# Optimization experiments

Measured on AMD Instinct MI355X. Metric: run time of the kernel, lower is better.

The kernel has to match this reference:

```python
import jax, jax.numpy as jnp
import numpy as np

H, P, T = 256, 16, 4      # hidden_size, maxout_pool_size, max_dec_steps
B, M = 32, 600            # batch, document length

def _lstm_cell(x, h, c, W_ih, W_hh, b_ih, b_hh):
    g = x @ W_ih.T + b_ih + h @ W_hh.T + b_hh
    i, f, gg, o = jnp.split(g, 4, axis=1)  # torch gate order i,f,g,o
    c = jax.nn.sigmoid(f) * c + jax.nn.sigmoid(i) * jnp.tanh(gg)
    h = jax.nn.sigmoid(o) * jnp.tanh(c)
    return h, c

def _maxout(h, U, u_cat, mask_mult, W_lin, W1, b1, W2, b2, W12, b12):
    b, m, _ = U.shape
    r = jnp.tanh(jnp.concatenate([h, u_cat], axis=1) @ W_lin.T)                  # [b,H]
    m1_in = jnp.concatenate([U, jnp.broadcast_to(r[:, None, :], (b, m, H))], 2)  # [b,m,3H]
    m1 = (m1_in @ W1.T + b1).reshape(b, m, H, P).max(-1)                         # [b,m,H]
    m2 = (m1 @ W2.T + b2).reshape(b, m, H, P).max(-1)                            # [b,m,H]
    alpha = (jnp.concatenate([m1, m2], axis=2) @ W12.T + b12).max(-1)            # [b,m]
    return jax.nn.log_softmax(alpha + mask_mult, axis=1)

def _forward(U, d_mask, span, W_ih, W_hh, b_ih, b_hh,
             Ws_lin, Ws_m1, bs_m1, Ws_m2, bs_m2, Ws_m12, bs_m12,
             We_lin, We_m1, be_m1, We_m2, be_m2, We_m12, be_m12):
    b, m, _ = U.shape
    idxb = jnp.arange(b)
    mask_mult = (1.0 - d_mask.astype(U.dtype)) * -1e30
    s_i = jnp.zeros(b, jnp.int32)
    e_i = (jnp.sum(d_mask, 1) - 1).astype(jnp.int32)
    s_tgt, e_tgt = span[:, 0], span[:, 1]
    h = jnp.zeros((b, H), U.dtype)
    c = jnp.zeros((b, H), U.dtype)
    mask_s = mask_e = None
    res_s, res_e, res_ms, res_me, losses = [], [], [], [], []
    u_s = U[idxb, s_i]
    for t in range(T):
        u_e = U[idxb, e_i]
        u_cat = jnp.concatenate([u_s, u_e], axis=1)
        h, c = _lstm_cell(u_cat, h, c, W_ih, W_hh, b_ih, b_hh)
        # start pointer
        lsm = _maxout(h, U, u_cat, mask_mult, Ws_lin, Ws_m1, bs_m1, Ws_m2, bs_m2, Ws_m12, bs_m12)
        idx = jnp.argmax(lsm, axis=1).astype(jnp.int32)
        if t == 0:
            mask_s = jnp.ones(b, bool)
        else:
            idx = idx * mask_s.astype(jnp.int32)
            prev = s_i * mask_s.astype(jnp.int32)
            mask_s = idx != prev
        loss_s = jnp.mean(-jnp.take_along_axis(lsm, s_tgt[:, None], 1)[:, 0]) * mask_s.astype(U.dtype)
        s_i = idx
        u_s = U[idxb, s_i]
        # end pointer
        u_cat2 = jnp.concatenate([u_s, u_e], axis=1)
        lsm_e = _maxout(h, U, u_cat2, mask_mult, We_lin, We_m1, be_m1, We_m2, be_m2, We_m12, be_m12)
        idx_e = jnp.argmax(lsm_e, axis=1).astype(jnp.int32)
        if t == 0:
            mask_e = jnp.ones(b, bool)
        else:
            idx_e = idx_e * mask_e.astype(jnp.int32)
            prev_e = e_i * mask_e.astype(jnp.int32)
            mask_e = idx_e != prev_e
        loss_e = jnp.mean(-jnp.take_along_axis(lsm_e, e_tgt[:, None], 1)[:, 0]) * mask_e.astype(U.dtype)
        e_i = idx_e
        losses.append(loss_s + loss_e)
        res_s.append(s_i); res_ms.append(mask_s)
        res_e.append(e_i); res_me.append(mask_e)
    pos_s = jnp.sum(jnp.stack(res_ms, 1).astype(jnp.int32), 1) - 1
    p1 = jnp.take_along_axis(jnp.stack(res_s, 1), pos_s[:, None], 1)[:, 0]
    pos_e = jnp.sum(jnp.stack(res_me, 1).astype(jnp.int32), 1) - 1
    p2 = jnp.take_along_axis(jnp.stack(res_e, 1), pos_e[:, None], 1)[:, 0]
    loss = jnp.mean(jnp.sum(jnp.stack(losses, 1), 1) / T)
    return loss, p1, p2

def setup_inputs():
    key = jax.random.key(0)
    ks = jax.random.split(key, 16)
    U = jax.random.normal(ks[0], (B, M, 2 * H), jnp.float32)
    lengths = jax.random.randint(ks[1], (B,), M // 2, M + 1)
    d_mask = (jnp.arange(M)[None, :] < lengths[:, None]).astype(jnp.int32)
    span = jax.random.randint(ks[2], (B, 2), 0, M // 2).astype(jnp.int32)
    def w(k, shape, fan_in):
        return (jax.random.normal(k, shape, jnp.float32) / np.float32(np.sqrt(fan_in)))
    b_ih = jnp.zeros(4 * H, jnp.float32).at[H:2 * H].set(1.0)  # forget-gate bias init
    params = {
        'W_ih': w(ks[3], (4 * H, 4 * H), 4 * H), 'W_hh': w(ks[4], (4 * H, H), H),
        'b_ih': b_ih, 'b_hh': jnp.zeros(4 * H, jnp.float32),
        'Ws_lin': w(ks[5], (H, 5 * H), 5 * H),
        'Ws_m1': w(ks[6], (H * P, 3 * H), 3 * H), 'bs_m1': jnp.zeros(H * P, jnp.float32),
        'Ws_m2': w(ks[7], (H * P, H), H), 'bs_m2': jnp.zeros(H * P, jnp.float32),
        'Ws_m12': w(ks[8], (P, 2 * H), 2 * H), 'bs_m12': jnp.zeros(P, jnp.float32),
        'We_lin': w(ks[9], (H, 5 * H), 5 * H),
        'We_m1': w(ks[10], (H * P, 3 * H), 3 * H), 'be_m1': jnp.zeros(H * P, jnp.float32),
        'We_m2': w(ks[11], (H * P, H), H), 'be_m2': jnp.zeros(H * P, jnp.float32),
        'We_m12': w(ks[12], (P, 2 * H), 2 * H), 'be_m12': jnp.zeros(P, jnp.float32),
    }
    return {'U': U, 'd_mask': d_mask, 'span': span, **params}

def reference(U, d_mask, span, W_ih, W_hh, b_ih, b_hh,
              Ws_lin, Ws_m1, bs_m1, Ws_m2, bs_m2, Ws_m12, bs_m12,
              We_lin, We_m1, be_m1, We_m2, be_m2, We_m12, be_m12):
    return _forward(U, d_mask, span, W_ih, W_hh, b_ih, b_hh,
                    Ws_lin, Ws_m1, bs_m1, Ws_m2, bs_m2, Ws_m12, bs_m12,
                    We_lin, We_m1, be_m1, We_m2, be_m2, We_m12, be_m12)
```

## Files before the change

### kernel.cpp

```cpp
#include <hip/hip_runtime.h>
#include <math.h>

namespace {

typedef unsigned short u16;
typedef __attribute__((ext_vector_type(4))) float f32x4;
typedef __attribute__((ext_vector_type(8))) _Float16 f16x8;
typedef __attribute__((ext_vector_type(4))) _Float16 f16x4;

constexpr int B = 32;
constexpr int M = 600;
constexpr int H = 256;
constexpr int TSTEPS = 4;
constexpr int HP = 4096;
constexpr int BM = B * M;
constexpr int TWOH = 512;
constexpr int THREEH = 768;
constexpr int FOURH = 1024;
constexpr int FIVEH = 1280;
constexpr int NTILES = BM / 128;

__device__ __forceinline__ float sigf(float x) { return 1.0f / (1.0f + expf(-x)); }

__device__ __forceinline__ void gload16(const u16* g, u16* l) {
    __builtin_amdgcn_global_load_lds(
        (const __attribute__((address_space(1))) void*)g,
        (__attribute__((address_space(3))) void*)l, 16, 0, 0);
}

__global__ void k_init(const int* __restrict__ d_mask,
                       float* __restrict__ h, float* __restrict__ c,
                       float* __restrict__ loss_vec,
                       int* __restrict__ s_i, int* __restrict__ e_i,
                       int* __restrict__ p1r, int* __restrict__ p2r)
{
    int tid = threadIdx.x;
    for (int i = tid; i < B * H; i += 256) { h[i] = 0.f; c[i] = 0.f; }
    if (tid < B) {
        loss_vec[tid] = 0.f;
        s_i[tid] = 0;
        int s = 0;
        const int* row = d_mask + tid * M;
        for (int m = 0; m < M; ++m) s += row[m];
        e_i[tid] = s - 1;
        p1r[tid] = 0; p2r[tid] = 0;
    }
}

__global__ __launch_bounds__(128) void k_flags(const int* __restrict__ d_mask,
                                               int* __restrict__ flags)
{
    int bm = blockIdx.x * 128 + threadIdx.x;
    int cnt = __syncthreads_count(d_mask[bm]);
    if (threadIdx.x == 0) flags[blockIdx.x] = (cnt == 0) ? 1 : 0;
}

__global__ __launch_bounds__(256) void k_gather(
    const float* __restrict__ U, const int* __restrict__ s_i,
    const int* __restrict__ e_i, float* __restrict__ u_cat)
{
    int idx = blockIdx.x * 256 + threadIdx.x;
    int b = idx >> 9, k = idx & 511;
    u_cat[b * FOURH + k]       = U[((size_t)b * M + s_i[b]) * TWOH + k];
    u_cat[b * FOURH + 512 + k] = U[((size_t)b * M + e_i[b]) * TWOH + k];
}

__global__ __launch_bounds__(256) void k_lstm_gemm(
    const float* __restrict__ u_cat, const float* __restrict__ h,
    const float* __restrict__ W_ih, const float* __restrict__ W_hh,
    const float* __restrict__ b_ih, const float* __restrict__ b_hh,
    float* __restrict__ g)
{
    int idx = blockIdx.x * 256 + threadIdx.x;
    int b = idx >> 10, j = idx & 1023;
    float acc = 0.f;
    const float4* x4 = (const float4*)(u_cat + b * FOURH);
    const float4* wi4 = (const float4*)(W_ih + (size_t)j * FOURH);
    #pragma unroll 4
    for (int k = 0; k < FOURH / 4; ++k) {
        float4 a = x4[k], w = wi4[k];
        acc += a.x * w.x + a.y * w.y + a.z * w.z + a.w * w.w;
    }
    const float4* h4 = (const float4*)(h + b * H);
    const float4* wh4 = (const float4*)(W_hh + (size_t)j * H);
    #pragma unroll 4
    for (int k = 0; k < H / 4; ++k) {
        float4 a = h4[k], w = wh4[k];
        acc += a.x * w.x + a.y * w.y + a.z * w.z + a.w * w.w;
    }
    g[idx] = acc + b_ih[j] + b_hh[j];
}

__global__ __launch_bounds__(256) void k_lstm_gates(
    const float* __restrict__ g, float* __restrict__ h, float* __restrict__ c)
{
    int idx = blockIdx.x * 256 + threadIdx.x;
    int b = idx >> 8, i = idx & (H - 1);
    const float* gr = g + b * FOURH;
    float gi = gr[i], gf = gr[H + i], gg = gr[2 * H + i], go = gr[3 * H + i];
    float cn = sigf(gf) * c[idx] + sigf(gi) * tanhf(gg);
    c[idx] = cn;
    h[idx] = sigf(go) * tanhf(cn);
}

__global__ __launch_bounds__(256) void k_r(
    const float* __restrict__ h, const float* __restrict__ u_cat,
    const float* __restrict__ W_lin, float* __restrict__ r)
{
    int idx = blockIdx.x * 256 + threadIdx.x;
    int b = idx >> 8, i = idx & (H - 1);
    const float* w = W_lin + (size_t)i * FIVEH;
    float acc = 0.f;
    const float4* h4 = (const float4*)(h + b * H);
    const float4* w4 = (const float4*)w;
    #pragma unroll 4
    for (int k = 0; k < H / 4; ++k) {
        float4 a = h4[k], ww = w4[k];
        acc += a.x * ww.x + a.y * ww.y + a.z * ww.z + a.w * ww.w;
    }
    const float4* x4 = (const float4*)(u_cat + b * FOURH);
    const float4* w4b = (const float4*)(w + H);
    #pragma unroll 4
    for (int k = 0; k < FOURH / 4; ++k) {
        float4 a = x4[k], ww = w4b[k];
        acc += a.x * ww.x + a.y * ww.y + a.z * ww.z + a.w * ww.w;
    }
    r[idx] = tanhf(acc);
}

__global__ __launch_bounds__(256) void k_rW(
    const float* __restrict__ r, const float* __restrict__ W1,
    const float* __restrict__ b1, float* __restrict__ rW)
{
    int idx = blockIdx.x * 256 + threadIdx.x;
    int b = idx >> 12, j = idx & (HP - 1);
    const float4* r4 = (const float4*)(r + b * H);
    const float4* w4 = (const float4*)(W1 + (size_t)j * THREEH + TWOH);
    float acc = 0.f;
    #pragma unroll 4
    for (int k = 0; k < H / 4; ++k) {
        float4 a = r4[k], w = w4[k];
        acc += a.x * w.x + a.y * w.y + a.z * w.z + a.w * w.w;
    }
    rW[idx] = acc + b1[j];
}

__global__ __launch_bounds__(256) void k_rW2(
    const float* __restrict__ r, const float* __restrict__ Wt,
    const float* __restrict__ b1, float* __restrict__ rW)
{
    const int b = blockIdx.y;
    const int j = blockIdx.x * 256 + threadIdx.x;
    __shared__ float sr[256];
    sr[threadIdx.x] = r[b * H + threadIdx.x];
    __syncthreads();
    float acc = b1[j];
    #pragma unroll 4
    for (int k = 0; k < H; ++k) acc += sr[k] * Wt[(size_t)k * HP + j];
    rW[(size_t)b * HP + j] = acc;
}

__global__ __launch_bounds__(256) void k_transp(
    const float* __restrict__ W, float* __restrict__ Wt)
{
    int idx = blockIdx.x * 256 + threadIdx.x;
    int k = idx >> 12, j = idx & (HP - 1);
    Wt[idx] = W[(size_t)j * THREEH + TWOH + k];
}

__global__ __launch_bounds__(256) void k_cvtH(
    const float* __restrict__ src, int ld, int Kc, _Float16* __restrict__ dst)
{
    int i4 = blockIdx.x * 256 + threadIdx.x;
    int perrow = Kc >> 2;
    int row = i4 / perrow;
    int kc = (i4 - row * perrow) << 2;
    float4 v = *(const float4*)(src + (size_t)row * ld + kc);
    f16x4 o;
    o[0] = (_Float16)v.x; o[1] = (_Float16)v.y; o[2] = (_Float16)v.z; o[3] = (_Float16)v.w;
    *(f16x4*)(dst + (size_t)row * Kc + kc) = o;
}

template <int EPI>
__global__ __launch_bounds__(256, 4) void gemmJ(
    const _Float16* __restrict__ A, const _Float16* __restrict__ Bw,
    int K, const float* __restrict__ extra, const int* __restrict__ skip,
    float* __restrict__ Cf, _Float16* __restrict__ Ch)
{
    if (skip[blockIdx.y]) return;
    __shared__ __align__(16) u16 sA[2][128 * 32];
    __shared__ __align__(16) u16 sB[2][128 * 32];
    const int tid = threadIdx.x;
    const int w = tid >> 6, lane = tid & 63;
    const int row0 = blockIdx.y * 128, col0 = blockIdx.x * 128;
    const int wm = w & 1, wn = w >> 1;

    const int r1g = tid >> 2,        k1 = (tid & 3) ^ ((r1g >> 1) & 3);
    const int r2g = (tid + 256) >> 2, k2 = ((tid + 256) & 3) ^ ((r2g >> 1) & 3);
    const size_t gA1 = (size_t)(row0 + r1g) * K + k1 * 8;
    const size_t gA2 = (size_t)(row0 + r2g) * K + k2 * 8;
    const size_t gB1 = (size_t)(col0 + r1g) * K + k1 * 8;
    const size_t gB2 = (size_t)(col0 + r2g) * K + k2 * 8;

    f32x4 acc[4][4] = {};

    gload16((const u16*)(A  + gA1), &sA[0][tid * 8]);
    gload16((const u16*)(A  + gA2), &sA[0][(tid + 256) * 8]);
    gload16((const u16*)(Bw + gB1), &sB[0][tid * 8]);
    gload16((const u16*)(Bw + gB2), &sB[0][(tid + 256) * 8]);

    const int iters = K >> 5;
    const int mrow = lane & 15;
    const int kg = lane >> 4;
    const int slot = kg ^ ((mrow >> 1) & 3);
    const int eoff = slot << 3;

    for (int it = 0; it < iters; ++it) {
        const int cur = it & 1;
        __syncthreads();
        if (it + 1 < iters) {
            const int k0n = (it + 1) << 5;
            gload16((const u16*)(A  + gA1 + k0n), &sA[1 - cur][tid * 8]);
            gload16((const u16*)(A  + gA2 + k0n), &sA[1 - cur][(tid + 256) * 8]);
            gload16((const u16*)(Bw + gB1 + k0n), &sB[1 - cur][tid * 8]);
            gload16((const u16*)(Bw + gB2 + k0n), &sB[1 - cur][(tid + 256) * 8]);
        }
        const u16* pa = &sA[cur][(wm * 64 + mrow) * 32 + eoff];
        const u16* pb = &sB[cur][(wn * 64 + mrow) * 32 + eoff];
        f16x8 fa[4], fb[4];
        #pragma unroll
        for (int f = 0; f < 4; ++f) {
            fa[f] = *(const f16x8*)(pa + f * 16 * 32);
            fb[f] = *(const f16x8*)(pb + f * 16 * 32);
        }
        #pragma unroll
        for (int i = 0; i < 4; ++i) {
            #pragma unroll
            for (int j = 0; j < 4; ++j) {
                acc[i][j] = __builtin_amdgcn_mfma_f32_16x16x32_f16(fa[i], fb[j], acc[i][j], 0, 0, 0);
            }
        }
    }

    const int cq = lane & 15, rq = lane >> 4;
    if (EPI == 4) {
        #pragma unroll
        for (int i = 0; i < 4; ++i) {
            #pragma unroll
            for (int j = 0; j < 4; ++j) {
                int col = col0 + wn * 64 + j * 16 + cq;
                #pragma unroll
                for (int rr = 0; rr < 4; ++rr) {
                    int row = row0 + wm * 64 + i * 16 + rq * 4 + rr;
                    Ch[(size_t)row * HP + col] = (_Float16)acc[i][j][rr];
                }
            }
        }
    } else if (EPI == 1) {
        #pragma unroll
        for (int j = 0; j < 4; ++j) {
            int col = col0 + wn * 64 + j * 16 + cq;
            int gcol = (col0 >> 4) + wn * 4 + j;
            float bv = extra[col];
            #pragma unroll
            for (int i = 0; i < 4; ++i) {
                #pragma unroll
                for (int rr = 0; rr < 4; ++rr) {
                    float v = acc[i][j][rr] + bv;
                    v = fmaxf(v, __shfl_xor(v, 1));
                    v = fmaxf(v, __shfl_xor(v, 2));
                    v = fmaxf(v, __shfl_xor(v, 4));
                    v = fmaxf(v, __shfl_xor(v, 8));
                    if (cq == 0) {
                        int row = row0 + wm * 64 + i * 16 + rq * 4 + rr;
                        Cf[(size_t)row * H + gcol] = v;
                    }
                }
            }
        }
    } else {
        #pragma unroll
        for (int j = 0; j < 4; ++j) {
            int col = col0 + wn * 64 + j * 16 + cq;
            int gcol = (col0 >> 4) + wn * 4 + j;
            #pragma unroll
            for (int i = 0; i < 4; ++i) {
                #pragma unroll
                for (int rr = 0; rr < 4; ++rr) {
                    int row = row0 + wm * 64 + i * 16 + rq * 4 + rr;
                    int b = row / M;
                    float v = acc[i][j][rr] + extra[(size_t)b * HP + col];
                    v = fmaxf(v, __shfl_xor(v, 1));
                    v = fmaxf(v, __shfl_xor(v, 2));
                    v = fmaxf(v, __shfl_xor(v, 4));
                    v = fmaxf(v, __shfl_xor(v, 8));
                    if (cq == 0)
                        Ch[(size_t)row * H + gcol] = (_Float16)v;
                }
            }
        }
    }
}

__global__ __launch_bounds__(256) void k_m1A16(
    const _Float16* __restrict__ A, const float* __restrict__ rW,
    _Float16* __restrict__ m1)
{
    int idx = blockIdx.x * 256 + threadIdx.x;
    int bm = idx >> 8;
    int h = idx & (H - 1);
    int b = bm / M;
    const f16x8* a8 = (const f16x8*)(A + (size_t)bm * HP + (h << 4));
    const float4* r4 = (const float4*)(rW + (size_t)b * HP + (h << 4));
    f16x8 a0 = a8[0], a1 = a8[1];
    float4 ra = r4[0], rb = r4[1], rc = r4[2], rd = r4[3];
    float mx;
    mx = fmaxf(fmaxf(fmaxf((float)a0[0] + ra.x, (float)a0[1] + ra.y),
                     fmaxf((float)a0[2] + ra.z, (float)a0[3] + ra.w)),
         fmaxf(fmaxf((float)a0[4] + rb.x, (float)a0[5] + rb.y),
               fmaxf((float)a0[6] + rb.z, (float)a0[7] + rb.w)));
    mx = fmaxf(mx,
         fmaxf(fmaxf(fmaxf((float)a1[0] + rc.x, (float)a1[1] + rc.y),
                     fmaxf((float)a1[2] + rc.z, (float)a1[3] + rc.w)),
               fmaxf(fmaxf((float)a1[4] + rd.x, (float)a1[5] + rd.y),
                     fmaxf((float)a1[6] + rd.z, (float)a1[7] + rd.w))));
    m1[idx] = (_Float16)mx;
}

template <int EPI>
__global__ __launch_bounds__(256) void gemm64(
    const float* __restrict__ Ag, int lda,
    const float* __restrict__ Bg, int ldb,
    const float* __restrict__ extra,
    float* __restrict__ C, int K, int ldc)
{
    __shared__ float As[16][68];
    __shared__ float Bs[16][68];
    const int tid = threadIdx.x;
    const int tx = tid & 15;
    const int ty = tid >> 4;
    const int row0 = blockIdx.y * 64;
    const int col0 = blockIdx.x * 64;
    const int lr = tid >> 2;
    const int lk = (tid & 3) << 2;
    const float* Aload = Ag + (size_t)(row0 + lr) * lda + lk;
    const float* Bload = Bg + (size_t)(col0 + lr) * ldb + lk;
    float acc[4][4] = {};
    for (int k0 = 0; k0 < K; k0 += 16) {
        float4 av = *(const float4*)(Aload + k0);
        float4 bv = *(const float4*)(Bload + k0);
        __syncthreads();
        As[lk + 0][lr] = av.x; As[lk + 1][lr] = av.y; As[lk + 2][lr] = av.z; As[lk + 3][lr] = av.w;
        Bs[lk + 0][lr] = bv.x; Bs[lk + 1][lr] = bv.y; Bs[lk + 2][lr] = bv.z; Bs[lk + 3][lr] = bv.w;
        __syncthreads();
        #pragma unroll
        for (int k = 0; k < 16; ++k) {
            float4 a4 = *(const float4*)(&As[k][ty << 2]);
            float4 b4 = *(const float4*)(&Bs[k][tx << 2]);
            acc[0][0] += a4.x * b4.x; acc[0][1] += a4.x * b4.y; acc[0][2] += a4.x * b4.z; acc[0][3] += a4.x * b4.w;
            acc[1][0] += a4.y * b4.x; acc[1][1] += a4.y * b4.y; acc[1][2] += a4.y * b4.z; acc[1][3] += a4.y * b4.w;
            acc[2][0] += a4.z * b4.x; acc[2][1] += a4.z * b4.y; acc[2][2] += a4.z * b4.z; acc[2][3] += a4.z * b4.w;
            acc[3][0] += a4.w * b4.x; acc[3][1] += a4.w * b4.y; acc[3][2] += a4.w * b4.z; acc[3][3] += a4.w * b4.w;
        }
    }
    if (EPI == 1) {
        const int cb = col0 + (tx << 2);
        float b0 = extra[cb], b1v = extra[cb + 1], b2v = extra[cb + 2], b3v = extra[cb + 3];
        #pragma unroll
        for (int i = 0; i < 4; ++i) {
            float mth = fmaxf(fmaxf(acc[i][0] + b0, acc[i][1] + b1v),
                              fmaxf(acc[i][2] + b2v, acc[i][3] + b3v));
            float r1 = fmaxf(mth, __shfl_xor(mth, 1));
            float r2 = fmaxf(r1, __shfl_xor(r1, 2));
            if ((tx & 3) == 0)
                C[(size_t)(row0 + (ty << 2) + i) * ldc + (col0 >> 4) + (tx >> 2)] = r2;
        }
    } else if (EPI == 2) {
        const int cb = col0 + (tx << 2);
        #pragma unroll
        for (int i = 0; i < 4; ++i) {
            int row = row0 + (ty << 2) + i;
            int b = row / M;
            const float* rw = extra + (size_t)b * HP + cb;
            float mth = fmaxf(fmaxf(acc[i][0] + rw[0], acc[i][1] + rw[1]),
                              fmaxf(acc[i][2] + rw[2], acc[i][3] + rw[3]));
            float r1 = fmaxf(mth, __shfl_xor(mth, 1));
            float r2 = fmaxf(r1, __shfl_xor(r1, 2));
            if ((tx & 3) == 0)
                C[(size_t)row * ldc + (col0 >> 4) + (tx >> 2)] = r2;
        }
    }
}

__global__ __launch_bounds__(256) void k_alpha(
    const float* __restrict__ m1, const float* __restrict__ m2,
    const float* __restrict__ W12, const float* __restrict__ b12,
    const int* __restrict__ d_mask, float* __restrict__ alpha)
{
    __shared__ float Ws[16 * 512];
    const int tid = threadIdx.x;
    for (int i = tid; i < 16 * 512; i += 256) Ws[i] = W12[i];
    __syncthreads();
    const int wave = tid >> 6, lane = tid & 63;
    const int bm = blockIdx.x * 4 + wave;
    const float* r1 = m1 + (size_t)bm * H;
    const float* r2 = m2 + (size_t)bm * H;
    float acc[16] = {};
    #pragma unroll
    for (int q = 0; q < 4; ++q) {
        int k = lane + (q << 6);
        float x = r1[k];
        #pragma unroll
        for (int p = 0; p < 16; ++p) acc[p] += x * Ws[p * 512 + k];
    }
    #pragma unroll
    for (int q = 0; q < 4; ++q) {
        int k = lane + (q << 6);
        float x = r2[k];
        #pragma unroll
        for (int p = 0; p < 16; ++p) acc[p] += x * Ws[p * 512 + 256 + k];
    }
    #pragma unroll
    for (int p = 0; p < 16; ++p) {
        float v = acc[p];
        v += __shfl_xor(v, 1);  v += __shfl_xor(v, 2);  v += __shfl_xor(v, 4);
        v += __shfl_xor(v, 8);  v += __shfl_xor(v, 16); v += __shfl_xor(v, 32);
        acc[p] = v;
    }
    if (lane == 0) {
        float mx = -INFINITY;
        #pragma unroll
        for (int p = 0; p < 16; ++p) mx = fmaxf(mx, acc[p] + b12[p]);
        alpha[bm] = d_mask[bm] ? mx : -1e30f;
    }
}

__global__ __launch_bounds__(256) void k_alpha2(
    const _Float16* __restrict__ m1, const float* __restrict__ m2,
    const float* __restrict__ W12, const float* __restrict__ b12,
    const int* __restrict__ d_mask, float* __restrict__ alpha)
{
    __shared__ float Ws[16 * 512];
    const int tid = threadIdx.x;
    for (int i = tid; i < 16 * 512; i += 256) Ws[i] = W12[i];
    __syncthreads();
    const int wave = tid >> 6, lane = tid & 63;
    const int bm = blockIdx.x * 4 + wave;
    if (!d_mask[bm]) {
        if (lane == 0) alpha[bm] = -1e30f;
        return;
    }
    const _Float16* r1 = m1 + (size_t)bm * H;
    const float* r2 = m2 + (size_t)bm * H;
    float acc[16] = {};
    #pragma unroll
    for (int q = 0; q < 4; ++q) {
        int k = lane + (q << 6);
        float x = (float)r1[k];
        #pragma unroll
        for (int p = 0; p < 16; ++p) acc[p] += x * Ws[p * 512 + k];
    }
    #pragma unroll
    for (int q = 0; q < 4; ++q) {
        int k = lane + (q << 6);
        float x = r2[k];
        #pragma unroll
        for (int p = 0; p < 16; ++p) acc[p] += x * Ws[p * 512 + 256 + k];
    }
    #pragma unroll
    for (int p = 0; p < 16; ++p) {
        float v = acc[p];
        v += __shfl_xor(v, 1);  v += __shfl_xor(v, 2);  v += __shfl_xor(v, 4);
        v += __shfl_xor(v, 8);  v += __shfl_xor(v, 16); v += __shfl_xor(v, 32);
        acc[p] = v;
    }
    if (lane == 0) {
        float mx = -INFINITY;
        #pragma unroll
        for (int p = 0; p < 16; ++p) mx = fmaxf(mx, acc[p] + b12[p]);
        alpha[bm] = mx;
    }
}

__global__ __launch_bounds__(256) void k_softmax(
    const float* __restrict__ alpha, const int* __restrict__ span, int phase,
    float* __restrict__ loss_term, int* __restrict__ idx_out)
{
    __shared__ float sv[256];
    __shared__ int si[256];
    const int b = blockIdx.x, tid = threadIdx.x;
    const float* row = alpha + b * M;
    float best = -INFINITY; int bidx = 0;
    for (int m = tid; m < M; m += 256) {
        float v = row[m];
        if (v > best) { best = v; bidx = m; }
    }
    sv[tid] = best; si[tid] = bidx;
    __syncthreads();
    for (int s = 128; s > 0; s >>= 1) {
        if (tid < s) {
            float v2 = sv[tid + s]; int i2 = si[tid + s];
            if (v2 > sv[tid] || (v2 == sv[tid] && i2 < si[tid])) { sv[tid] = v2; si[tid] = i2; }
        }
        __syncthreads();
    }
    float bmax = sv[0]; int amax = si[0];
    __syncthreads();
    float ps = 0.f;
    for (int m = tid; m < M; m += 256) ps += expf(row[m] - bmax);
    sv[tid] = ps;
    __syncthreads();
    for (int s = 128; s > 0; s >>= 1) {
        if (tid < s) sv[tid] += sv[tid + s];
        __syncthreads();
    }
    if (tid == 0) {
        float lse = bmax + logf(sv[0]);
        int tgt = span[b * 2 + phase];
        loss_term[b] = -(row[tgt] - lse);
        idx_out[b] = amax;
    }
}

__global__ void k_update(const int* __restrict__ idx_in, const float* __restrict__ loss_term,
                         int* __restrict__ pos, int* __restrict__ mask,
                         int* __restrict__ prun, float* __restrict__ loss_vec, int t)
{
    int b = threadIdx.x;
    int active = (b < B) ? 1 : 0;
    int ni = 0, nm = 0;
    if (active) {
        int id = idx_in[b];
        if (t == 0) { nm = 1; ni = id; }
        else {
            int om = mask[b];
            ni = id * om;
            int prev = pos[b] * om;
            nm = (ni != prev) ? 1 : 0;
        }
    }
    float v = active ? loss_term[b] : 0.f;
    #pragma unroll
    for (int off = 32; off > 0; off >>= 1) v += __shfl_xor(v, off);
    float S = v * (1.0f / (float)B);
    if (active) {
        pos[b] = ni;
        mask[b] = nm;
        if (nm) { prun[b] = ni; loss_vec[b] += S; }
    }
}

__global__ void k_finalize(const float* __restrict__ loss_vec, const int* __restrict__ p1r,
                           const int* __restrict__ p2r, float* __restrict__ out)
{
    int b = threadIdx.x;
    float v = (b < B) ? loss_vec[b] : 0.f;
    #pragma unroll
    for (int off = 32; off > 0; off >>= 1) v += __shfl_xor(v, off);
    if (b == 0) out[0] = v / (float)(B * TSTEPS);
    if (b < B) {
        out[1 + b] = (float)p1r[b];
        out[1 + B + b] = (float)p2r[b];
    }
}

}

extern "C" void kernel_launch(void* const* d_in, const int* in_sizes, int n_in,
                              void* d_out, int out_size, void* d_ws, size_t ws_size,
                              hipStream_t stream)
{
    const float* U      = (const float*)d_in[0];
    const int*   d_mask = (const int*)d_in[1];
    const int*   span   = (const int*)d_in[2];
    const float* W_ih   = (const float*)d_in[3];
    const float* W_hh   = (const float*)d_in[4];
    const float* b_ih   = (const float*)d_in[5];
    const float* b_hh   = (const float*)d_in[6];
    const float* Ws_lin = (const float*)d_in[7];
    const float* Ws_m1  = (const float*)d_in[8];
    const float* bs_m1  = (const float*)d_in[9];
    const float* Ws_m2  = (const float*)d_in[10];
    const float* bs_m2  = (const float*)d_in[11];
    const float* Ws_m12 = (const float*)d_in[12];
    const float* bs_m12 = (const float*)d_in[13];
    const float* We_lin = (const float*)d_in[14];
    const float* We_m1  = (const float*)d_in[15];
    const float* be_m1  = (const float*)d_in[16];
    const float* We_m2  = (const float*)d_in[17];
    const float* be_m2  = (const float*)d_in[18];
    const float* We_m12 = (const float*)d_in[19];
    const float* be_m12 = (const float*)d_in[20];

    float* ws = (float*)d_ws;
    size_t o = 0;
    float* m2b   = ws + o; o += (size_t)BM * H;
    float* alphab= ws + o; o += BM;
    float* u_cat = ws + o; o += B * FOURH;
    float* gbuf  = ws + o; o += B * FOURH;
    float* hbuf  = ws + o; o += B * H;
    float* cbuf  = ws + o; o += B * H;
    float* rbuf  = ws + o; o += B * H;
    float* rWb   = ws + o; o += B * HP;
    float* loss_term = ws + o; o += B;
    float* loss_vec  = ws + o; o += B;
    int* ib = (int*)(ws + o); o += 8 * B + 160;
    int* idxb   = ib + 0 * B;
    int* s_i    = ib + 1 * B;
    int* e_i    = ib + 2 * B;
    int* mask_s = ib + 3 * B;
    int* mask_e = ib + 4 * B;
    int* p1r    = ib + 5 * B;
    int* p2r    = ib + 6 * B;
    int* flags  = ib + 8 * B;
    size_t o_common = (o + 3) & ~(size_t)3;

    float* m1b = ws + o_common;

    size_t p = o_common;
    float* Wt_s = ws + p; p += (size_t)H * HP;
    float* Wt_e = ws + p; p += (size_t)H * HP;
    _Float16* hs = (_Float16*)(ws + p);
    size_t q = 0;
    _Float16* Uh  = hs + q; q += (size_t)BM * TWOH;
    _Float16* W1s = hs + q; q += (size_t)HP * TWOH;
    _Float16* W1e = hs + q; q += (size_t)HP * TWOH;
    _Float16* W2s = hs + q; q += (size_t)HP * H;
    _Float16* W2e = hs + q; q += (size_t)HP * H;
    _Float16* m1b16 = hs + q; q += (size_t)BM * H;
    q = (q + 7) & ~(size_t)7;
    const size_t need2 = p * sizeof(float) + q * sizeof(_Float16);
    _Float16* A_s16 = hs + q;
    _Float16* A_e16 = A_s16 + (size_t)BM * HP;
    const size_t need15s = need2 + (size_t)BM * HP * sizeof(_Float16);
    const size_t need16  = need15s + (size_t)BM * HP * sizeof(_Float16);

    const int tier = (ws_size >= need16) ? 16
                   : (ws_size >= need15s) ? 15
                   : (ws_size >= need2) ? 2 : 3;

    k_init<<<1, 256, 0, stream>>>(d_mask, hbuf, cbuf, loss_vec, s_i, e_i, p1r, p2r);

    if (tier != 3) {
        k_flags<<<NTILES, 128, 0, stream>>>(d_mask, flags);
        k_cvtH<<<BM * TWOH / 4 / 256, 256, 0, stream>>>(U, TWOH, TWOH, Uh);
        k_cvtH<<<HP * TWOH / 4 / 256, 256, 0, stream>>>(Ws_m1, THREEH, TWOH, W1s);
        k_cvtH<<<HP * TWOH / 4 / 256, 256, 0, stream>>>(We_m1, THREEH, TWOH, W1e);
        k_cvtH<<<HP * H / 4 / 256, 256, 0, stream>>>(Ws_m2, H, H, W2s);
        k_cvtH<<<HP * H / 4 / 256, 256, 0, stream>>>(We_m2, H, H, W2e);
        k_transp<<<HP * H / 256, 256, 0, stream>>>(Ws_m1, Wt_s);
        k_transp<<<HP * H / 256, 256, 0, stream>>>(We_m1, Wt_e);

        dim3 gJ(HP / 128, NTILES);
        if (tier >= 15) {
            gemmJ<4><<<gJ, 256, 0, stream>>>(Uh, W1s, TWOH, nullptr, flags, nullptr, A_s16);
        }
        if (tier == 16) {
            gemmJ<4><<<gJ, 256, 0, stream>>>(Uh, W1e, TWOH, nullptr, flags, nullptr, A_e16);
        }

        for (int t = 0; t < TSTEPS; ++t) {
            k_gather<<<64, 256, 0, stream>>>(U, s_i, e_i, u_cat);
            k_lstm_gemm<<<128, 256, 0, stream>>>(u_cat, hbuf, W_ih, W_hh, b_ih, b_hh, gbuf);
            k_lstm_gates<<<32, 256, 0, stream>>>(gbuf, hbuf, cbuf);

            k_r<<<32, 256, 0, stream>>>(hbuf, u_cat, Ws_lin, rbuf);
            k_rW2<<<dim3(HP / 256, B), 256, 0, stream>>>(rbuf, Wt_s, bs_m1, rWb);
            if (tier >= 15)
                k_m1A16<<<BM * H / 256, 256, 0, stream>>>(A_s16, rWb, m1b16);
            else
                gemmJ<3><<<gJ, 256, 0, stream>>>(Uh, W1s, TWOH, rWb, flags, nullptr, m1b16);
            gemmJ<1><<<gJ, 256, 0, stream>>>(m1b16, W2s, H, bs_m2, flags, m2b, nullptr);
            k_alpha2<<<BM / 4, 256, 0, stream>>>(m1b16, m2b, Ws_m12, bs_m12, d_mask, alphab);
            k_softmax<<<B, 256, 0, stream>>>(alphab, span, 0, loss_term, idxb);
            k_update<<<1, 64, 0, stream>>>(idxb, loss_term, s_i, mask_s, p1r, loss_vec, t);

            k_gather<<<64, 256, 0, stream>>>(U, s_i, e_i, u_cat);

            k_r<<<32, 256, 0, stream>>>(hbuf, u_cat, We_lin, rbuf);
            k_rW2<<<dim3(HP / 256, B), 256, 0, stream>>>(rbuf, Wt_e, be_m1, rWb);
            if (tier == 16)
                k_m1A16<<<BM * H / 256, 256, 0, stream>>>(A_e16, rWb, m1b16);
            else
                gemmJ<3><<<gJ, 256, 0, stream>>>(Uh, W1e, TWOH, rWb, flags, nullptr, m1b16);
            gemmJ<1><<<gJ, 256, 0, stream>>>(m1b16, W2e, H, be_m2, flags, m2b, nullptr);
            k_alpha2<<<BM / 4, 256, 0, stream>>>(m1b16, m2b, We_m12, be_m12, d_mask, alphab);
            k_softmax<<<B, 256, 0, stream>>>(alphab, span, 1, loss_term, idxb);
            k_update<<<1, 64, 0, stream>>>(idxb, loss_term, e_i, mask_e, p2r, loss_vec, t);
        }
    } else {
        dim3 gemm_grid(HP / 64, BM / 64);
        for (int t = 0; t < TSTEPS; ++t) {
            k_gather<<<64, 256, 0, stream>>>(U, s_i, e_i, u_cat);
            k_lstm_gemm<<<128, 256, 0, stream>>>(u_cat, hbuf, W_ih, W_hh, b_ih, b_hh, gbuf);
            k_lstm_gates<<<32, 256, 0, stream>>>(gbuf, hbuf, cbuf);

            k_r<<<32, 256, 0, stream>>>(hbuf, u_cat, Ws_lin, rbuf);
            k_rW<<<512, 256, 0, stream>>>(rbuf, Ws_m1, bs_m1, rWb);
            gemm64<2><<<gemm_grid, 256, 0, stream>>>(U, TWOH, Ws_m1, THREEH, rWb, m1b, TWOH, H);
            gemm64<1><<<gemm_grid, 256, 0, stream>>>(m1b, H, Ws_m2, H, bs_m2, m2b, H, H);
            k_alpha<<<BM / 4, 256, 0, stream>>>(m1b, m2b, Ws_m12, bs_m12, d_mask, alphab);
            k_softmax<<<B, 256, 0, stream>>>(alphab, span, 0, loss_term, idxb);
            k_update<<<1, 64, 0, stream>>>(idxb, loss_term, s_i, mask_s, p1r, loss_vec, t);

            k_gather<<<64, 256, 0, stream>>>(U, s_i, e_i, u_cat);

            k_r<<<32, 256, 0, stream>>>(hbuf, u_cat, We_lin, rbuf);
            k_rW<<<512, 256, 0, stream>>>(rbuf, We_m1, be_m1, rWb);
            gemm64<2><<<gemm_grid, 256, 0, stream>>>(U, TWOH, We_m1, THREEH, rWb, m1b, TWOH, H);
            gemm64<1><<<gemm_grid, 256, 0, stream>>>(m1b, H, We_m2, H, be_m2, m2b, H, H);
            k_alpha<<<BM / 4, 256, 0, stream>>>(m1b, m2b, We_m12, be_m12, d_mask, alphab);
            k_softmax<<<B, 256, 0, stream>>>(alphab, span, 1, loss_term, idxb);
            k_update<<<1, 64, 0, stream>>>(idxb, loss_term, e_i, mask_e, p2r, loss_vec, t);
        }
    }

    k_finalize<<<1, 64, 0, stream>>>(loss_vec, p1r, p2r, (float*)d_out);
}
```

Baseline: 2.884 ms.

## Fuse gather into LSTM/r kernels, merge softmax+update, batch alpha rows per wave

Removes the separate gather launches by reading the U rows at s_i/e_i directly inside new LSTM-GEMM and r kernels. Softmax, argmax and the pointer/loss update are merged into a single 1024-thread block kernel, one wave per batch row. k_alpha2 now handles four rows per wave, so its launch shrinks and the W12 shared-memory load is spread over more rows. This cuts kernel launches and redundant W12 staging. The cost is a single-block reduction kernel and less parallelism in the alpha kernel.

Result: no change. 2.878 ms (-0.2%).

```diff
diff --git a/kernel.cpp b/kernel.cpp
--- a/kernel.cpp
+++ b/kernel.cpp
@@ -65,6 +65,42 @@
     u_cat[b * FOURH + 512 + k] = U[((size_t)b * M + e_i[b]) * TWOH + k];
 }
 
+__global__ __launch_bounds__(256) void k_lstm_gemm2(
+    const float* __restrict__ U, const int* __restrict__ s_i,
+    const int* __restrict__ e_i, const float* __restrict__ h,
+    const float* __restrict__ W_ih, const float* __restrict__ W_hh,
+    const float* __restrict__ b_ih, const float* __restrict__ b_hh,
+    float* __restrict__ g)
+{
+    int idx = blockIdx.x * 256 + threadIdx.x;
+    int b = idx >> 10, j = idx & 1023;
+    const float* us = U + ((size_t)b * M + s_i[b]) * TWOH;
+    const float* ue = U + ((size_t)b * M + e_i[b]) * TWOH;
+    float acc = 0.f;
+    const float4* x4 = (const float4*)us;
+    const float4* wi4 = (const float4*)(W_ih + (size_t)j * FOURH);
+    #pragma unroll 4
+    for (int k = 0; k < TWOH / 4; ++k) {
+        float4 a = x4[k], w = wi4[k];
+        acc += a.x * w.x + a.y * w.y + a.z * w.z + a.w * w.w;
+    }
+    const float4* y4 = (const float4*)ue;
+    const float4* wi4b = wi4 + TWOH / 4;
+    #pragma unroll 4
+    for (int k = 0; k < TWOH / 4; ++k) {
+        float4 a = y4[k], w = wi4b[k];
+        acc += a.x * w.x + a.y * w.y + a.z * w.z + a.w * w.w;
+    }
+    const float4* h4 = (const float4*)(h + b * H);
+    const float4* wh4 = (const float4*)(W_hh + (size_t)j * H);
+    #pragma unroll 4
+    for (int k = 0; k < H / 4; ++k) {
+        float4 a = h4[k], w = wh4[k];
+        acc += a.x * w.x + a.y * w.y + a.z * w.z + a.w * w.w;
+    }
+    g[idx] = acc + b_ih[j] + b_hh[j];
+}
+
 __global__ __launch_bounds__(256) void k_lstm_gemm(
     const float* __restrict__ u_cat, const float* __restrict__ h,
     const float* __restrict__ W_ih, const float* __restrict__ W_hh,
@@ -101,6 +137,39 @@
     float cn = sigf(gf) * c[idx] + sigf(gi) * tanhf(gg);
     c[idx] = cn;
     h[idx] = sigf(go) * tanhf(cn);
+}
+
+__global__ __launch_bounds__(256) void k_r2(
+    const float* __restrict__ h, const float* __restrict__ U,
+    const int* __restrict__ s_i, const int* __restrict__ e_i,
+    const float* __restrict__ W_lin, float* __restrict__ r)
+{
+    int idx = blockIdx.x * 256 + threadIdx.x;
+    int b = idx >> 8, i = idx & (H - 1);
+    const float* w = W_lin + (size_t)i * FIVEH;
+    float acc = 0.f;
+    const float4* h4 = (const float4*)(h + b * H);
+    const float4* w4 = (const float4*)w;
+    #pragma unroll 4
+    for (int k = 0; k < H / 4; ++k) {
+        float4 a = h4[k], ww = w4[k];
+        acc += a.x * ww.x + a.y * ww.y + a.z * ww.z + a.w * ww.w;
+    }
+    const float4* x4 = (const float4*)(U + ((size_t)b * M + s_i[b]) * TWOH);
+    const float4* w4b = (const float4*)(w + H);
+    #pragma unroll 4
+    for (int k = 0; k < TWOH / 4; ++k) {
+        float4 a = x4[k], ww = w4b[k];
+        acc += a.x * ww.x + a.y * ww.y + a.z * ww.z + a.w * ww.w;
+    }
+    const float4* y4 = (const float4*)(U + ((size_t)b * M + e_i[b]) * TWOH);
+    const float4* w4c = (const float4*)(w + H + TWOH);
+    #pragma unroll 4
+    for (int k = 0; k < TWOH / 4; ++k) {
+        float4 a = y4[k], ww = w4c[k];
+        acc += a.x * ww.x + a.y * ww.y + a.z * ww.z + a.w * ww.w;
+    }
+    r[idx] = tanhf(acc);
 }
 
 __global__ __launch_bounds__(256) void k_r(
@@ -445,40 +514,102 @@
     for (int i = tid; i < 16 * 512; i += 256) Ws[i] = W12[i];
     __syncthreads();
     const int wave = tid >> 6, lane = tid & 63;
-    const int bm = blockIdx.x * 4 + wave;
-    if (!d_mask[bm]) {
-        if (lane == 0) alpha[bm] = -1e30f;
-        return;
-    }
-    const _Float16* r1 = m1 + (size_t)bm * H;
-    const float* r2 = m2 + (size_t)bm * H;
-    float acc[16] = {};
-    #pragma unroll
-    for (int q = 0; q < 4; ++q) {
-        int k = lane + (q << 6);
-        float x = (float)r1[k];
-        #pragma unroll
-        for (int p = 0; p < 16; ++p) acc[p] += x * Ws[p * 512 + k];
-    }
-    #pragma unroll
-    for (int q = 0; q < 4; ++q) {
-        int k = lane + (q << 6);
-        float x = r2[k];
-        #pragma unroll
-        for (int p = 0; p < 16; ++p) acc[p] += x * Ws[p * 512 + 256 + k];
-    }
-    #pragma unroll
-    for (int p = 0; p < 16; ++p) {
-        float v = acc[p];
-        v += __shfl_xor(v, 1);  v += __shfl_xor(v, 2);  v += __shfl_xor(v, 4);
-        v += __shfl_xor(v, 8);  v += __shfl_xor(v, 16); v += __shfl_xor(v, 32);
-        acc[p] = v;
-    }
-    if (lane == 0) {
-        float mx = -INFINITY;
-        #pragma unroll
-        for (int p = 0; p < 16; ++p) mx = fmaxf(mx, acc[p] + b12[p]);
-        alpha[bm] = mx;
+    const int bm0 = blockIdx.x * 16 + wave * 4;
+    for (int rr = 0; rr < 4; ++rr) {
+        const int bm = bm0 + rr;
+        if (!d_mask[bm]) {
+            if (lane == 0) alpha[bm] = -1e30f;
+            continue;
+        }
+        const _Float16* r1 = m1 + (size_t)bm * H;
+        const float* r2 = m2 + (size_t)bm * H;
+        float acc[16] = {};
+        #pragma unroll
+        for (int q = 0; q < 4; ++q) {
+            int k = lane + (q << 6);
+            float x = (float)r1[k];
+            #pragma unroll
+            for (int p = 0; p < 16; ++p) acc[p] += x * Ws[p * 512 + k];
+        }
+        #pragma unroll
+        for (int q = 0; q < 4; ++q) {
+            int k = lane + (q << 6);
+            float x = r2[k];
+            #pragma unroll
+            for (int p = 0; p < 16; ++p) acc[p] += x * Ws[p * 512 + 256 + k];
+        }
+        #pragma unroll
+        for (int p = 0; p < 16; ++p) {
+            float v = acc[p];
+            v += __shfl_xor(v, 1);  v += __shfl_xor(v, 2);  v += __shfl_xor(v, 4);
+            v += __shfl_xor(v, 8);  v += __shfl_xor(v, 16); v += __shfl_xor(v, 32);
+            acc[p] = v;
+        }
+        if (lane == 0) {
+            float mx = -INFINITY;
+            #pragma unroll
+            for (int p = 0; p < 16; ++p) mx = fmaxf(mx, acc[p] + b12[p]);
+            alpha[bm] = mx;
+        }
+    }
+}
+
+__global__ __launch_bounds__(1024) void k_smu(
+    const float* __restrict__ alpha, const int* __restrict__ span, int phase,
+    int* __restrict__ pos, int* __restrict__ mask,
+    int* __restrict__ prun, float* __restrict__ loss_vec, int t)
+{
+    __shared__ float s_loss[B];
+    __shared__ int s_idx[B];
+    const int wave = threadIdx.x >> 6, lane = threadIdx.x & 63;
+    for (int b = wave; b < B; b += 16) {
+        const float* row = alpha + b * M;
+        float best = -INFINITY; int bidx = 0;
+        for (int m = lane; m < M; m += 64) {
+            float v = row[m];
+            if (v > best) { best = v; bidx = m; }
+        }
+        #pragma unroll
+        for (int off = 1; off < 64; off <<= 1) {
+            float v2 = __shfl_xor(best, off);
+            int i2 = __shfl_xor(bidx, off);
+            if (v2 > best || (v2 == best && i2 < bidx)) { best = v2; bidx = i2; }
+        }
+        float ps = 0.f;
+        for (int m = lane; m < M; m += 64) ps += expf(row[m] - best);
+        #pragma unroll
+        for (int off = 32; off > 0; off >>= 1) ps += __shfl_xor(ps, off);
+        if (lane == 0) {
+            float lse = best + logf(ps);
+            int tgt = span[b * 2 + phase];
+            s_loss[b] = -(row[tgt] - lse);
+            s_idx[b] = bidx;
+        }
+    }
+    __syncthreads();
+    if (wave == 0) {
+        int b = lane;
+        int active = (b < B) ? 1 : 0;
+        int ni = 0, nm = 0;
+        if (active) {
+            int id = s_idx[b];
+            if (t == 0) { nm = 1; ni = id; }
+            else {
+                int om = mask[b];
+                ni = id * om;
+                int prev = pos[b] * om;
+                nm = (ni != prev) ? 1 : 0;
+            }
+        }
+        float v = active ? s_loss[b] : 0.f;
+        #pragma unroll
+        for (int off = 32; off > 0; off >>= 1) v += __shfl_xor(v, off);
+        float S = v * (1.0f / (float)B);
+        if (active) {
+            pos[b] = ni;
+            mask[b] = nm;
+            if (nm) { prun[b] = ni; loss_vec[b] += S; }
+        }
     }
 }
 
@@ -660,33 +791,28 @@
         }
 
         for (int t = 0; t < TSTEPS; ++t) {
-            k_gather<<<64, 256, 0, stream>>>(U, s_i, e_i, u_cat);
-            k_lstm_gemm<<<128, 256, 0, stream>>>(u_cat, hbuf, W_ih, W_hh, b_ih, b_hh, gbuf);
+            k_lstm_gemm2<<<128, 256, 0, stream>>>(U, s_i, e_i, hbuf, W_ih, W_hh, b_ih, b_hh, gbuf);
             k_lstm_gates<<<32, 256, 0, stream>>>(gbuf, hbuf, cbuf);
 
-            k_r<<<32, 256, 0, stream>>>(hbuf, u_cat, Ws_lin, rbuf);
+            k_r2<<<32, 256, 0, stream>>>(hbuf, U, s_i, e_i, Ws_lin, rbuf);
             k_rW2<<<dim3(HP / 256, B), 256, 0, stream>>>(rbuf, Wt_s, bs_m1, rWb);
             if (tier >= 15)
                 k_m1A16<<<BM * H / 256, 256, 0, stream>>>(A_s16, rWb, m1b16);
             else
                 gemmJ<3><<<gJ, 256, 0, stream>>>(Uh, W1s, TWOH, rWb, flags, nullptr, m1b16);
             gemmJ<1><<<gJ, 256, 0, stream>>>(m1b16, W2s, H, bs_m2, flags, m2b, nullptr);
-            k_alpha2<<<BM / 4, 256, 0, stream>>>(m1b16, m2b, Ws_m12, bs_m12, d_mask, alphab);
-            k_softmax<<<B, 256, 0, stream>>>(alphab, span, 0, loss_term, idxb);
-            k_update<<<1, 64, 0, stream>>>(idxb, loss_term, s_i, mask_s, p1r, loss_vec, t);
-
-            k_gather<<<64, 256, 0, stream>>>(U, s_i, e_i, u_cat);
-
-            k_r<<<32, 256, 0, stream>>>(hbuf, u_cat, We_lin, rbuf);
+            k_alpha2<<<BM / 16, 256, 0, stream>>>(m1b16, m2b, Ws_m12, bs_m12, d_mask, alphab);
+            k_smu<<<1, 1024, 0, stream>>>(alphab, span, 0, s_i, mask_s, p1r, loss_vec, t);
+
+            k_r2<<<32, 256, 0, stream>>>(hbuf, U, s_i, e_i, We_lin, rbuf);
             k_rW2<<<dim3(HP / 256, B), 256, 0, stream>>>(rbuf, Wt_e, be_m1, rWb);
             if (tier == 16)
                 k_m1A16<<<BM * H / 256, 256, 0, stream>>>(A_e16, rWb, m1b16);
             else
                 gemmJ<3><<<gJ, 256, 0, stream>>>(Uh, W1e, TWOH, rWb, flags, nullptr, m1b16);
             gemmJ<1><<<gJ, 256, 0, stream>>>(m1b16, W2e, H, be_m2, flags, m2b, nullptr);
-            k_alpha2<<<BM / 4, 256, 0, stream>>>(m1b16, m2b, We_m12, be_m12, d_mask, alphab);
-            k_softmax<<<B, 256, 0, stream>>>(alphab, span, 1, loss_term, idxb);
-            k_update<<<1, 64, 0, stream>>>(idxb, loss_term, e_i, mask_e, p2r, loss_vec, t);
+            k_alpha2<<<BM / 16, 256, 0, stream>>>(m1b16, m2b, We_m12, be_m12, d_mask, alphab);
+            k_smu<<<1, 1024, 0, stream>>>(alphab, span, 1, e_i, mask_e, p2r, loss_vec, t);
         }
     } else {
         dim3 gemm_grid(HP / 64, BM / 64);
```
